# Optimization experiments

Hardware: AMD Instinct MI355X
Metric: run time of the kernel (lower is better)

Reference implementation:

```python
import math
import jax, jax.numpy as jnp
import numpy as np


def setup_inputs() -> dict:
    key = jax.random.key(0)
    k1, k2 = jax.random.split(key)
    bs, n_heads, ch, T, ratio = 2, 4, 64, 1024, 4
    q = jax.random.normal(k1, (bs, n_heads * ch, T), dtype=jnp.float32)
    kv = jax.random.normal(k2, (bs, n_heads * 2 * ch, T * ratio), dtype=jnp.float32)
    return {"q": q, "kv": kv, "n_heads": n_heads}


def reference(q, kv, n_heads):
    bs, width, length = q.shape
    _, _, length_kv = kv.shape
    ch = width // n_heads
    B = bs * n_heads
    s = int(math.isqrt(length))            # spatial side, length == s*s
    ratio = length_kv // length

    qh = q.reshape(B, ch, s, s).astype(jnp.float32)
    k_, v_ = jnp.split(kv.reshape(B, 2 * ch, length_kv), 2, axis=1)

    # 2-D FFT + fftshift on q and k
    qf = jnp.fft.fftshift(jnp.fft.fftn(qh, axes=(-2, -1)), axes=(-2, -1))
    qf = qf.reshape(B, ch, length)                      # complex64 [B, ch, T]
    kh = k_.reshape(B, ch, ratio, s, s).astype(jnp.float32)
    kf = jnp.fft.fftshift(jnp.fft.fftn(kh, axes=(-2, -1)), axes=(-2, -1))
    kf = kf.reshape(B, ch, length_kv)                   # complex64 [B, ch, T_kv]

    scale = 1.0 / math.sqrt(math.sqrt(ch))
    w = jnp.einsum('bct,bcs->bts', qf * scale, kf * scale)  # complex [B, T, T_kv]

    # softmax over kv axis, applied separately to real and imag parts
    wr = jnp.stack([w.real, w.imag], axis=-1)           # [B, T, T_kv, 2]
    wr = jax.nn.softmax(wr, axis=-2)
    w = jax.lax.complex(wr[..., 0], wr[..., 1])

    # inverse shift + inverse 2-D FFT, keep real part
    w = w.reshape(B, length, ratio, s, s)
    w = jnp.fft.ifftn(jnp.fft.ifftshift(w, axes=(-2, -1)), axes=(-2, -1)).real
    w = w.reshape(B, length, length_kv).astype(kv.dtype)

    a = jnp.einsum('bts,bcs->bct', w, v_)               # [B, ch, T]
    return a.reshape(bs, n_heads * ch, length)
```

## Files before the change

### kernel.cpp

```cpp
#include <hip/hip_runtime.h>
#include <math.h>

typedef _Float16 half8 __attribute__((ext_vector_type(8)));
typedef float f32x16 __attribute__((ext_vector_type(16)));

#define L2E 1.4426950408889634f
#define KPLANE (8*4096*64)
#define QPLANE (8*1024*64)
#define VPLANE (8*64*4096)

__device__ constexpr float FW_R[16] = {
  1.0f, 0.98078528040323044f, 0.92387953251128674f, 0.83146961230254524f,
  0.70710678118654757f, 0.55557023301960218f, 0.38268343236508978f, 0.19509032201612825f,
  0.0f, -0.19509032201612825f, -0.38268343236508978f, -0.55557023301960218f,
  -0.70710678118654757f, -0.83146961230254524f, -0.92387953251128674f, -0.98078528040323044f };
__device__ constexpr float FW_I[16] = {
  -0.0f, -0.19509032201612825f, -0.38268343236508978f, -0.55557023301960218f,
  -0.70710678118654757f, -0.83146961230254524f, -0.92387953251128674f, -0.98078528040323044f,
  -1.0f, -0.98078528040323044f, -0.92387953251128674f, -0.83146961230254524f,
  -0.70710678118654757f, -0.55557023301960218f, -0.38268343236508978f, -0.19509032201612825f };

static __device__ __forceinline__ void fft32(float* xr, float* xi) {
  #pragma unroll
  for (int i = 0; i < 32; i++) {
    int j = ((i & 1) << 4) | ((i & 2) << 2) | (i & 4) | ((i >> 2) & 2) | ((i >> 4) & 1);
    if (j > i) {
      float t = xr[i]; xr[i] = xr[j]; xr[j] = t;
      t = xi[i]; xi[i] = xi[j]; xi[j] = t;
    }
  }
  #pragma unroll
  for (int s = 1; s <= 5; s++) {
    const int len = 1 << s, half = len >> 1;
    #pragma unroll
    for (int j0 = 0; j0 < 32; j0 += len) {
      #pragma unroll
      for (int k = 0; k < half; k++) {
        const float wr = FW_R[k << (5 - s)], wi = FW_I[k << (5 - s)];
        const int a = j0 + k, b = a + half;
        float tr = xr[b] * wr - xi[b] * wi;
        float ti = xr[b] * wi + xi[b] * wr;
        xr[b] = xr[a] - tr; xi[b] = xi[a] - ti;
        xr[a] += tr; xi[a] += ti;
      }
    }
  }
}

__global__ __launch_bounds__(256) void fft2_all(
    const float* __restrict__ q, const float* __restrict__ kv,
    _Float16* __restrict__ KrH, _Float16* __restrict__ KrL,
    _Float16* __restrict__ KiH, _Float16* __restrict__ KiL,
    _Float16* __restrict__ QrH, _Float16* __restrict__ QrL,
    _Float16* __restrict__ QiH, _Float16* __restrict__ QiL,
    _Float16* __restrict__ Vre, _Float16* __restrict__ Vim)
{
  __shared__ float2 G[8 * 1057];
  const int blk = blockIdx.x;
  const int tid = threadIdx.x;
  const int tr = tid >> 5, col = tid & 31;
  int mode, idx;
  if (blk < 64)       { mode = 0; idx = blk; }
  else if (blk < 320) { mode = 1; idx = blk - 64; }
  else                { mode = 2; idx = blk - 320; }
  int co, r, b;
  if (mode == 0) { co = idx & 7; r = 0;              b = idx >> 3; }
  else           { co = idx & 7; r = (idx >> 3) & 3; b = idx >> 5; }
  const int c = co * 8 + tr;
  const float* src;
  int src_off;
  float scale;
  if (mode == 0)      { src = q;  src_off = (b * 64 + c) * 1024;                  scale = 0.35355339059327373f * L2E; }
  else if (mode == 1) { src = kv; src_off = (b * 128 + c) * 4096 + r * 1024;      scale = 0.35355339059327373f; }
  else                { src = kv; src_off = (b * 128 + 64 + c) * 4096 + r * 1024; scale = 1.0f / 1024.0f; }

  float2* Gt = &G[tr * 1057];

  float xr[32], xi[32];
  #pragma unroll
  for (int n1 = 0; n1 < 32; n1++) { xr[n1] = src[src_off + n1 * 32 + col]; xi[n1] = 0.f; }
  fft32(xr, xi);
  #pragma unroll
  for (int u1 = 0; u1 < 32; u1++) Gt[col * 33 + u1] = make_float2(xr[u1], xi[u1]);
  __syncthreads();

  #pragma unroll
  for (int n2 = 0; n2 < 32; n2++) {
    float2 g = Gt[n2 * 33 + col];
    xr[n2] = g.x; xi[n2] = g.y;
  }
  fft32(xr, xi);
  float* yre = xr;
  float* yim = xi;

  const int su1 = (col + 16) & 31;
  if (mode == 2) {
    int o = (b * 64 + c) * 4096 + r * 1024 + su1 * 32;
    half8 hr[4], hi[4];
    #pragma unroll
    for (int g8 = 0; g8 < 4; g8++)
      #pragma unroll
      for (int e = 0; e < 8; e++) {
        int u2 = ((g8 * 8 + e) + 16) & 31;
        hr[g8][e] = (_Float16)(yre[u2] * scale);
        hi[g8][e] = (_Float16)(yim[u2] * scale);
      }
    #pragma unroll
    for (int g8 = 0; g8 < 4; g8++) {
      *(half8*)(Vre + o + g8 * 8) = hr[g8];
      *(half8*)(Vim + o + g8 * 8) = hi[g8];
    }
  } else {
    __syncthreads();
    #pragma unroll
    for (int u2 = 0; u2 < 32; u2++) {
      int su2 = (u2 + 16) & 31;
      Gt[su1 * 33 + su2] = make_float2(yre[u2] * scale, yim[u2] * scale);
    }
    __syncthreads();
    _Float16 *p0, *p1, *p2, *p3;
    int obase;
    if (mode == 0) { p0 = QrH; p1 = QrL; p2 = QiH; p3 = QiL; obase = (b * 1024) * 64 + co * 8; }
    else           { p0 = KrH; p1 = KrL; p2 = KiH; p3 = KiL; obase = (b * 4096 + r * 1024) * 64 + co * 8; }
    #pragma unroll 2
    for (int k = 0; k < 4; k++) {
      int p = tid + k * 256;
      int pl = (p >> 5) * 33 + (p & 31);
      half8 vH, vL, wH, wL;
      #pragma unroll
      for (int t8 = 0; t8 < 8; t8++) {
        float2 yv = G[t8 * 1057 + pl];
        _Float16 rh = (_Float16)yv.x;
        _Float16 ih = (_Float16)yv.y;
        vH[t8] = rh; vL[t8] = (_Float16)(yv.x - (float)rh);
        wH[t8] = ih; wL[t8] = (_Float16)(yv.y - (float)ih);
      }
      int o = obase + p * 64;
      *(half8*)(p0 + o) = vH;
      *(half8*)(p1 + o) = vL;
      *(half8*)(p2 + o) = wH;
      *(half8*)(p3 + o) = wL;
    }
  }
}

static __device__ inline void storeP(unsigned* pb, const float* p, int lh) {
  #pragma unroll
  for (int u = 0; u < 8; u++) {
    int base = ((u & 1) * 2) + ((u >> 1) * 8) + 4 * lh;
    unsigned short h0 = __builtin_bit_cast(unsigned short, (_Float16)p[2 * u]);
    unsigned short h1 = __builtin_bit_cast(unsigned short, (_Float16)p[2 * u + 1]);
    pb[base >> 1] = (unsigned)h0 | ((unsigned)h1 << 16);
  }
}
static __device__ inline half8 loadP(const unsigned* rp) {
  union { uint4 u; half8 h; } U;
  U.u = *(const uint4*)rp;
  return U.h;
}

__global__ __launch_bounds__(512, 2) void attn_mfma(
    const _Float16* __restrict__ KrH, const _Float16* __restrict__ KrL,
    const _Float16* __restrict__ KiH, const _Float16* __restrict__ KiL,
    const _Float16* __restrict__ QrH, const _Float16* __restrict__ QrL,
    const _Float16* __restrict__ QiH, const _Float16* __restrict__ QiL,
    const _Float16* __restrict__ Vre, const _Float16* __restrict__ Vim,
    float* __restrict__ out)
{
  __shared__ __align__(16) _Float16 qlds[4][4][64][8];
  __shared__ __align__(16) unsigned pbuf[8][32][20];
  __shared__ float mlb[8][32][5];
  __shared__ float obuf[8][32][33];

  const int tid = threadIdx.x;
  const int lane = tid & 63;
  const int warp = tid >> 6;
  const int b = blockIdx.x & 7;
  const int t0 = (blockIdx.x >> 3) << 5;
  const int lm = lane & 31, lh = lane >> 5;

  {
    const _Float16* qp[4] = {QrH, QrL, QiH, QiL};
    #pragma unroll
    for (int jj = 0; jj < 2; jj++) {
      int idx = tid + jj * 512;
      int pl = idx >> 8, ks = (idx >> 6) & 3, ln = idx & 63;
      int t = ln & 31, hh = ln >> 5;
      const _Float16* s = qp[pl] + ((b * 1024 + t0 + t) * 64 + ks * 16 + hh * 8);
      *(half8*)&qlds[pl][ks][ln][0] = *(const half8*)s;
    }
  }
  __syncthreads();

  int kbase = (b * 4096 + warp * 512 + lm) * 64 + lh * 8;
  const int vbase0 = (b * 64 + lm) * 4096 + warp * 512 + lh * 8;
  const int vbase1 = vbase0 + 32 * 4096;

  float m_r = -3e38f, m_i = -3e38f, l_r = 0.f, l_i = 0.f;
  f32x16 Or0 = (f32x16)(0.0f), Or1 = (f32x16)(0.0f);
  f32x16 Oi0 = (f32x16)(0.0f), Oi1 = (f32x16)(0.0f);

  #pragma unroll 1
  for (int it = 0; it < 16; ++it) {
    f32x16 A1 = (f32x16)(0.0f), A2 = (f32x16)(0.0f), SI = (f32x16)(0.0f);
    #pragma unroll
    for (int ks = 0; ks < 4; ks++) {
      half8 qrh = *(const half8*)&qlds[0][ks][lane][0];
      half8 qrl = *(const half8*)&qlds[1][ks][lane][0];
      half8 qih = *(const half8*)&qlds[2][ks][lane][0];
      half8 qil = *(const half8*)&qlds[3][ks][lane][0];
      const int ko = kbase + ks * 16;
      half8 krh = *(const half8*)(KrH + ko);
      half8 krl = *(const half8*)(KrL + ko);
      half8 kih = *(const half8*)(KiH + ko);
      half8 kil = *(const half8*)(KiL + ko);
      A1 = __builtin_amdgcn_mfma_f32_32x32x16_f16(krh, qrh, A1, 0, 0, 0);
      A2 = __builtin_amdgcn_mfma_f32_32x32x16_f16(kih, qih, A2, 0, 0, 0);
      SI = __builtin_amdgcn_mfma_f32_32x32x16_f16(kih, qrh, SI, 0, 0, 0);
      A1 = __builtin_amdgcn_mfma_f32_32x32x16_f16(krh, qrl, A1, 0, 0, 0);
      A2 = __builtin_amdgcn_mfma_f32_32x32x16_f16(kih, qil, A2, 0, 0, 0);
      SI = __builtin_amdgcn_mfma_f32_32x32x16_f16(krh, qih, SI, 0, 0, 0);
      A1 = __builtin_amdgcn_mfma_f32_32x32x16_f16(krl, qrh, A1, 0, 0, 0);
      A2 = __builtin_amdgcn_mfma_f32_32x32x16_f16(kil, qih, A2, 0, 0, 0);
      SI = __builtin_amdgcn_mfma_f32_32x32x16_f16(kil, qrh, SI, 0, 0, 0);
      SI = __builtin_amdgcn_mfma_f32_32x32x16_f16(kih, qrl, SI, 0, 0, 0);
      SI = __builtin_amdgcn_mfma_f32_32x32x16_f16(krl, qih, SI, 0, 0, 0);
      SI = __builtin_amdgcn_mfma_f32_32x32x16_f16(krh, qil, SI, 0, 0, 0);
    }

    float sre[16], sim[16];
    #pragma unroll
    for (int rr = 0; rr < 16; rr++) { sre[rr] = A1[rr] - A2[rr]; sim[rr] = SI[rr]; }

    float mtr = sre[0], mti = sim[0];
    #pragma unroll
    for (int rr = 1; rr < 16; rr++) { mtr = fmaxf(mtr, sre[rr]); mti = fmaxf(mti, sim[rr]); }
    mtr = fmaxf(mtr, __shfl_xor(mtr, 32));
    mti = fmaxf(mti, __shfl_xor(mti, 32));

    float pr[16], pi[16];
    {
      float mn = fmaxf(m_r, mtr);
      if (__ballot(mtr > m_r + 11.5f)) {
        float al = exp2f(m_r - mn);
        l_r *= al; m_r = mn;
        #pragma unroll
        for (int rr = 0; rr < 16; rr++) { Or0[rr] *= al; Or1[rr] *= al; }
      }
      float sm = 0.f;
      #pragma unroll
      for (int rr = 0; rr < 16; rr++) { pr[rr] = exp2f(sre[rr] - m_r); sm += pr[rr]; }
      l_r += sm + __shfl_xor(sm, 32);
    }
    {
      float mn = fmaxf(m_i, mti);
      if (__ballot(mti > m_i + 11.5f)) {
        float al = exp2f(m_i - mn);
        l_i *= al; m_i = mn;
        #pragma unroll
        for (int rr = 0; rr < 16; rr++) { Oi0[rr] *= al; Oi1[rr] *= al; }
      }
      float sm = 0.f;
      #pragma unroll
      for (int rr = 0; rr < 16; rr++) { pi[rr] = exp2f(sim[rr] - m_i); sm += pi[rr]; }
      l_i += sm + __shfl_xor(sm, 32);
    }

    storeP(&pbuf[warp][lm][0], pr, lh);
    #pragma unroll
    for (int h = 0; h < 2; h++) {
      half8 pfr = loadP(&pbuf[warp][lm][h * 8 + 4 * lh]);
      const int vo = it * 32 + h * 16;
      half8 v0r = *(const half8*)(Vre + vbase0 + vo);
      half8 v1r = *(const half8*)(Vre + vbase1 + vo);
      Or0 = __builtin_amdgcn_mfma_f32_32x32x16_f16(v0r, pfr, Or0, 0, 0, 0);
      Or1 = __builtin_amdgcn_mfma_f32_32x32x16_f16(v1r, pfr, Or1, 0, 0, 0);
    }
    storeP(&pbuf[warp][lm][0], pi, lh);
    #pragma unroll
    for (int h = 0; h < 2; h++) {
      half8 pfi = loadP(&pbuf[warp][lm][h * 8 + 4 * lh]);
      const int vo = it * 32 + h * 16;
      half8 v0i = *(const half8*)(Vim + vbase0 + vo);
      half8 v1i = *(const half8*)(Vim + vbase1 + vo);
      Oi0 = __builtin_amdgcn_mfma_f32_32x32x16_f16(v0i, pfi, Oi0, 0, 0, 0);
      Oi1 = __builtin_amdgcn_mfma_f32_32x32x16_f16(v1i, pfi, Oi1, 0, 0, 0);
    }
    kbase += 32 * 64;
  }

  if (lane < 32) {
    mlb[warp][lane][0] = m_r; mlb[warp][lane][1] = l_r;
    mlb[warp][lane][2] = m_i; mlb[warp][lane][3] = l_i;
  }
  __syncthreads();
  float Mr = -3e38f, Mi = -3e38f;
  #pragma unroll
  for (int w = 0; w < 8; w++) {
    Mr = fmaxf(Mr, mlb[w][lm][0]);
    Mi = fmaxf(Mi, mlb[w][lm][2]);
  }
  float Lr = 0.f, Li = 0.f;
  #pragma unroll
  for (int w = 0; w < 8; w++) {
    Lr += mlb[w][lm][1] * exp2f(mlb[w][lm][0] - Mr);
    Li += mlb[w][lm][3] * exp2f(mlb[w][lm][2] - Mi);
  }
  const float fr = exp2f(m_r - Mr) / Lr;
  const float fi = exp2f(m_i - Mi) / Li;

  #pragma unroll
  for (int rr = 0; rr < 16; rr++) {
    int cl = (rr & 3) + 8 * (rr >> 2) + 4 * lh;
    obuf[warp][cl][lm] = Or0[rr] * fr + Oi0[rr] * fi;
  }
  __syncthreads();
  {
    int c = tid >> 4, t2 = (tid & 15) * 2;
    float2 acc = make_float2(0.f, 0.f);
    #pragma unroll
    for (int w = 0; w < 8; w++) { acc.x += obuf[w][c][t2]; acc.y += obuf[w][c][t2 + 1]; }
    *(float2*)&out[(b * 64 + c) * 1024 + t0 + t2] = acc;
  }
  __syncthreads();
  #pragma unroll
  for (int rr = 0; rr < 16; rr++) {
    int cl = (rr & 3) + 8 * (rr >> 2) + 4 * lh;
    obuf[warp][cl][lm] = Or1[rr] * fr + Oi1[rr] * fi;
  }
  __syncthreads();
  {
    int c = tid >> 4, t2 = (tid & 15) * 2;
    float2 acc = make_float2(0.f, 0.f);
    #pragma unroll
    for (int w = 0; w < 8; w++) { acc.x += obuf[w][c][t2]; acc.y += obuf[w][c][t2 + 1]; }
    *(float2*)&out[(b * 64 + 32 + c) * 1024 + t0 + t2] = acc;
  }
}

extern "C" void kernel_launch(void* const* d_in, const int* in_sizes, int n_in,
                              void* d_out, int out_size, void* d_ws, size_t ws_size,
                              hipStream_t stream) {
  const float* q  = (const float*)d_in[0];
  const float* kv = (const float*)d_in[1];
  _Float16* base = (_Float16*)d_ws;
  _Float16* KrH = base;
  _Float16* KrL = KrH + KPLANE;
  _Float16* KiH = KrL + KPLANE;
  _Float16* KiL = KiH + KPLANE;
  _Float16* QrH = KiL + KPLANE;
  _Float16* QrL = QrH + QPLANE;
  _Float16* QiH = QrL + QPLANE;
  _Float16* QiL = QiH + QPLANE;
  _Float16* Vre = QiL + QPLANE;
  _Float16* Vim = Vre + VPLANE;
  float* out = (float*)d_out;

  fft2_all<<<576, 256, 0, stream>>>(q, kv, KrH, KrL, KiH, KiL,
                                    QrH, QrL, QiH, QiL, Vre, Vim);
  attn_mfma<<<256, 512, 0, stream>>>(KrH, KrL, KiH, KiL,
                                     QrH, QrL, QiH, QiL, Vre, Vim, out);
}
```

Before: 121.6 us.

## Split attention KV axis across two blocks and merge with a combine kernel

Splits the KV sequence into two halves so the attention kernel launches 512 blocks instead of 256. Each block writes fp16 partial outputs plus its softmax max and sum statistics to workspace. A new combine kernel rescales and merges the two halves into the final output. This raises occupancy and parallelism across the CUs, at the cost of an extra launch, extra global traffic, and fp16 rounding of the partial results.

```diff
diff --git a/kernel.cpp b/kernel.cpp
--- a/kernel.cpp
+++ b/kernel.cpp
@@ -2,12 +2,14 @@
 #include <math.h>
 
 typedef _Float16 half8 __attribute__((ext_vector_type(8)));
+typedef _Float16 half2t __attribute__((ext_vector_type(2)));
 typedef float f32x16 __attribute__((ext_vector_type(16)));
 
 #define L2E 1.4426950408889634f
 #define KPLANE (8*4096*64)
 #define QPLANE (8*1024*64)
 #define VPLANE (8*64*4096)
+#define PSZ 4352
 
 __device__ constexpr float FW_R[16] = {
   1.0f, 0.98078528040323044f, 0.92387953251128674f, 0.83146961230254524f,
@@ -165,7 +167,7 @@
     const _Float16* __restrict__ QrH, const _Float16* __restrict__ QrL,
     const _Float16* __restrict__ QiH, const _Float16* __restrict__ QiL,
     const _Float16* __restrict__ Vre, const _Float16* __restrict__ Vim,
-    float* __restrict__ out)
+    _Float16* __restrict__ part)
 {
   __shared__ __align__(16) _Float16 qlds[4][4][64][8];
   __shared__ __align__(16) unsigned pbuf[8][32][20];
@@ -176,7 +178,10 @@
   const int lane = tid & 63;
   const int warp = tid >> 6;
   const int b = blockIdx.x & 7;
-  const int t0 = (blockIdx.x >> 3) << 5;
+  const int tt = (blockIdx.x >> 3) & 31;
+  const int t0 = tt << 5;
+  const int shalf = blockIdx.x >> 8;
+  const int s0 = shalf << 11;
   const int lm = lane & 31, lh = lane >> 5;
 
   {
@@ -192,8 +197,8 @@
   }
   __syncthreads();
 
-  int kbase = (b * 4096 + warp * 512 + lm) * 64 + lh * 8;
-  const int vbase0 = (b * 64 + lm) * 4096 + warp * 512 + lh * 8;
+  int kbase = (b * 4096 + s0 + warp * 256 + lm) * 64 + lh * 8;
+  const int vbase0 = (b * 64 + lm) * 4096 + s0 + warp * 256 + lh * 8;
   const int vbase1 = vbase0 + 32 * 4096;
 
   float m_r = -3e38f, m_i = -3e38f, l_r = 0.f, l_i = 0.f;
@@ -201,7 +206,7 @@
   f32x16 Oi0 = (f32x16)(0.0f), Oi1 = (f32x16)(0.0f);
 
   #pragma unroll 1
-  for (int it = 0; it < 16; ++it) {
+  for (int it = 0; it < 8; ++it) {
     f32x16 A1 = (f32x16)(0.0f), A2 = (f32x16)(0.0f), SI = (f32x16)(0.0f);
     #pragma unroll
     for (int ks = 0; ks < 4; ks++) {
@@ -309,33 +314,73 @@
   const float fr = exp2f(m_r - Mr) / Lr;
   const float fi = exp2f(m_i - Mi) / Li;
 
-  #pragma unroll
-  for (int rr = 0; rr < 16; rr++) {
-    int cl = (rr & 3) + 8 * (rr >> 2) + 4 * lh;
-    obuf[warp][cl][lm] = Or0[rr] * fr + Oi0[rr] * fi;
+  const int pidx = (b * 32 + tt) * 2 + shalf;
+  _Float16* pO = part + pidx * PSZ;
+  float* pH = (float*)(pO + 4096);
+
+  #pragma unroll 1
+  for (int pass = 0; pass < 4; pass++) {
+    __syncthreads();
+    #pragma unroll
+    for (int rr = 0; rr < 16; rr++) {
+      int cl = (rr & 3) + 8 * (rr >> 2) + 4 * lh;
+      float v = (pass == 0) ? Or0[rr] * fr : (pass == 1) ? Or1[rr] * fr
+              : (pass == 2) ? Oi0[rr] * fi : Oi1[rr] * fi;
+      obuf[warp][cl][lm] = v;
+    }
+    __syncthreads();
+    {
+      int cc = tid >> 4, t2 = (tid & 15) * 2;
+      float a0 = 0.f, a1 = 0.f;
+      #pragma unroll
+      for (int w = 0; w < 8; w++) { a0 += obuf[w][cc][t2]; a1 += obuf[w][cc][t2 + 1]; }
+      int ofs = ((pass & 1) ? (32 + cc) : cc) * 32 + ((pass >> 1) ? 2048 : 0);
+      half2t hv; hv[0] = (_Float16)a0; hv[1] = (_Float16)a1;
+      *(half2t*)&pO[ofs + t2] = hv;
+    }
+  }
+  if (warp == 0 && lane < 32) {
+    pH[lane] = Mr; pH[32 + lane] = Lr; pH[64 + lane] = Mi; pH[96 + lane] = Li;
+  }
+}
+
+__global__ __launch_bounds__(256) void combine(
+    const _Float16* __restrict__ part, float* __restrict__ out)
+{
+  const int bt = blockIdx.x;
+  const int b = bt >> 5, tt = bt & 31;
+  const _Float16* p0 = part + (bt * 2) * PSZ;
+  const _Float16* p1 = p0 + PSZ;
+  const float* h0 = (const float*)(p0 + 4096);
+  const float* h1 = (const float*)(p1 + 4096);
+  __shared__ float wr0[32], wr1[32], wi0[32], wi1[32];
+  const int tid = threadIdx.x;
+  if (tid < 32) {
+    float m0 = h0[tid], m1 = h1[tid];
+    float M = fmaxf(m0, m1);
+    float g0 = exp2f(m0 - M) * h0[32 + tid], g1 = exp2f(m1 - M) * h1[32 + tid];
+    float iW = 1.f / (g0 + g1);
+    wr0[tid] = g0 * iW; wr1[tid] = g1 * iW;
+    m0 = h0[64 + tid]; m1 = h1[64 + tid];
+    M = fmaxf(m0, m1);
+    g0 = exp2f(m0 - M) * h0[96 + tid]; g1 = exp2f(m1 - M) * h1[96 + tid];
+    iW = 1.f / (g0 + g1);
+    wi0[tid] = g0 * iW; wi1[tid] = g1 * iW;
   }
   __syncthreads();
-  {
-    int c = tid >> 4, t2 = (tid & 15) * 2;
-    float2 acc = make_float2(0.f, 0.f);
-    #pragma unroll
-    for (int w = 0; w < 8; w++) { acc.x += obuf[w][c][t2]; acc.y += obuf[w][c][t2 + 1]; }
-    *(float2*)&out[(b * 64 + c) * 1024 + t0 + t2] = acc;
-  }
-  __syncthreads();
-  #pragma unroll
-  for (int rr = 0; rr < 16; rr++) {
-    int cl = (rr & 3) + 8 * (rr >> 2) + 4 * lh;
-    obuf[warp][cl][lm] = Or1[rr] * fr + Oi1[rr] * fi;
-  }
-  __syncthreads();
-  {
-    int c = tid >> 4, t2 = (tid & 15) * 2;
-    float2 acc = make_float2(0.f, 0.f);
-    #pragma unroll
-    for (int w = 0; w < 8; w++) { acc.x += obuf[w][c][t2]; acc.y += obuf[w][c][t2 + 1]; }
-    *(float2*)&out[(b * 64 + 32 + c) * 1024 + t0 + t2] = acc;
-  }
+  const int c = tid >> 2, tg = (tid & 3) * 8;
+  const int ob = (b * 64 + c) * 1024 + tt * 32 + tg;
+  float o[8];
+  #pragma unroll
+  for (int k = 0; k < 8; k++) {
+    int t = tg + k;
+    int e = c * 32 + t;
+    o[k] = (float)p0[e] * wr0[t] + (float)p1[e] * wr1[t]
+         + (float)p0[2048 + e] * wi0[t] + (float)p1[2048 + e] * wi1[t];
+  }
+  #pragma unroll
+  for (int k = 0; k < 8; k += 4)
+    *(float4*)&out[ob + k] = make_float4(o[k], o[k + 1], o[k + 2], o[k + 3]);
 }
 
 extern "C" void kernel_launch(void* const* d_in, const int* in_sizes, int n_in,
@@ -354,10 +399,12 @@
   _Float16* QiL = QiH + QPLANE;
   _Float16* Vre = QiL + QPLANE;
   _Float16* Vim = Vre + VPLANE;
+  _Float16* part = Vim + VPLANE;
   float* out = (float*)d_out;
 
   fft2_all<<<576, 256, 0, stream>>>(q, kv, KrH, KrL, KiH, KiL,
                                     QrH, QrL, QiH, QiL, Vre, Vim);
-  attn_mfma<<<256, 512, 0, stream>>>(KrH, KrL, KiH, KiL,
-                                     QrH, QrL, QiH, QiL, Vre, Vim, out);
-}
+  attn_mfma<<<512, 512, 0, stream>>>(KrH, KrL, KiH, KiL,
+                                     QrH, QrL, QiH, QiL, Vre, Vim, part);
+  combine<<<256, 256, 0, stream>>>(part, out);
+}
```

Result: slower. 134.6 us (+10.7%).
